# Kernel optimization log

Measured on AMD Instinct MI355X. Metric: run time of the kernel, lower is better.

The kernel has to match this reference:

```python
import jax, jax.numpy as jnp
import numpy as np

N = 100000      # nodes
E = 600000      # edges
IN = 128        # in_dim
HID = 32        # hidden_dim per head (layer 1)
HEADS = 4       # num_heads (layer 1)
NEG_SLOPE = 0.2 # PyG GATConv default negative_slope


def setup_inputs() -> dict:
    key = jax.random.key(0)
    ks = jax.random.split(key, 10)
    x = jax.random.normal(ks[0], (N, IN), dtype=jnp.float32)
    edge_index = jax.random.randint(ks[1], (2, E), 0, N, dtype=jnp.int64)
    # layer 1 params: W1 [IN, HEADS*HID], attention vectors [HEADS, HID], bias [HEADS*HID]
    W1 = jax.random.normal(ks[2], (IN, HEADS * HID), dtype=jnp.float32) / np.float32(np.sqrt(IN))
    att_src1 = jax.random.normal(ks[3], (HEADS, HID), dtype=jnp.float32) * 0.1
    att_dst1 = jax.random.normal(ks[4], (HEADS, HID), dtype=jnp.float32) * 0.1
    b1 = jnp.zeros((HEADS * HID,), dtype=jnp.float32)
    # layer 2 params: heads=1, out channels=1, concat=False
    W2 = jax.random.normal(ks[5], (HEADS * HID, 1), dtype=jnp.float32) / np.float32(np.sqrt(HEADS * HID))
    att_src2 = jax.random.normal(ks[6], (1, 1), dtype=jnp.float32) * 0.1
    att_dst2 = jax.random.normal(ks[7], (1, 1), dtype=jnp.float32) * 0.1
    b2 = jnp.zeros((1,), dtype=jnp.float32)
    return {"x": x, "edge_index": edge_index, "W1": W1, "att_src1": att_src1,
            "att_dst1": att_dst1, "b1": b1, "W2": W2, "att_src2": att_src2,
            "att_dst2": att_dst2, "b2": b2}


def gat_layer(x, src, dst, W, a_src, a_dst, b, heads, ch, concat):
    """PyG GATConv (eval mode): edge score + segment softmax + scatter aggregate."""
    n = x.shape[0]
    h = (x @ W).reshape(n, heads, ch)                    # [N,H,C]
    e_src = jnp.einsum('nhc,hc->nh', h, a_src)           # alpha_src per node
    e_dst = jnp.einsum('nhc,hc->nh', h, a_dst)           # alpha_dst per node
    e = jax.nn.leaky_relu(e_src[src] + e_dst[dst], NEG_SLOPE)  # [E,H]
    m = jax.ops.segment_max(e, dst, num_segments=n)      # stable softmax per dst
    p = jnp.exp(e - m[dst])
    denom = jax.ops.segment_sum(p, dst, num_segments=n)
    alpha = p / (denom[dst] + 1e-16)                     # [E,H]
    out = jax.ops.segment_sum(alpha[:, :, None] * h[src], dst, num_segments=n)  # [N,H,C]
    out = out.reshape(n, heads * ch) if concat else out.mean(axis=1)
    return out + b


def reference(x, edge_index, W1, att_src1, att_dst1, b1, W2, att_src2, att_dst2, b2):
    n = x.shape[0]
    loops = jnp.arange(n, dtype=edge_index.dtype)        # PyG add_self_loops=True
    src = jnp.concatenate([edge_index[0], loops])
    dst = jnp.concatenate([edge_index[1], loops])
    h1 = gat_layer(x, src, dst, W1, att_src1, att_dst1, b1, HEADS, HID, True)   # [N, HEADS*HID]
    out = gat_layer(h1, src, dst, W2, att_src2, att_dst2, b2, 1, 1, False)      # [N, 1]
    return out
```

## Files before the change

### kernel.cpp

```cpp
#include <hip/hip_runtime.h>
#include <hip/hip_fp16.h>
#include <math.h>

#define N_NODES 100000
#define E_EDGES 600000
#define IN_DIM  128
#define HID     32
#define HEADS   4
#define NEG     0.2f
#define CAP     32

typedef __attribute__((ext_vector_type(8))) _Float16 f16x8;
typedef __attribute__((ext_vector_type(4))) float f32x4;

__device__ __forceinline__ float lrelu(float v) { return v > 0.f ? v : NEG * v; }

#define SWZ(r, byteoff) ((byteoff) ^ (((r) & 7) << 4))


__global__ __launch_bounds__(128) void wprep_kernel(const float* __restrict__ W1,
                                                    const float* __restrict__ as1,
                                                    const float* __restrict__ ad1,
                                                    __half* __restrict__ wtx,
                                                    int* __restrict__ cnt) {
    int tid = blockIdx.x * 128 + threadIdx.x;
    for (int i = tid; i < N_NODES; i += 144 * 128) cnt[i] = 0;

    int b = blockIdx.x;
    int t = threadIdx.x;
    float v;
    if (b < 128) {
        v = W1[t * 128 + b];
    } else if (b < 136) {
        int h = b - 128;
        int hh = h & 3;
        const float* av = (h < 4) ? (as1 + hh * 32) : (ad1 + hh * 32);
        float s = 0.f;
        #pragma unroll 8
        for (int c = 0; c < 32; ++c) s += W1[t * 128 + hh * 32 + c] * av[c];
        v = s;
    } else {
        v = 0.f;
    }
    wtx[b * 128 + t] = __float2half(v);
}


__global__ __launch_bounds__(256) void gemm1_kernel(const float* __restrict__ x,
                                                    const __half* __restrict__ wtx,
                                                    __half* __restrict__ h1h,
                                                    float* __restrict__ aab) {
    __shared__ __half lx[64 * 128];
    __shared__ __half lw[144 * 128];
    int t = threadIdx.x;
    int row0 = blockIdx.x * 64;

    #pragma unroll
    for (int it = 0; it < 9; ++it) {
        int idx = t + it * 256;
        int r = idx >> 4, c = idx & 15;
        uint4 v = ((const uint4*)wtx)[idx];
        *(uint4*)((char*)lw + SWZ(r, r * 256 + c * 16)) = v;
    }
    #pragma unroll
    for (int it = 0; it < 8; ++it) {
        int idx = t + it * 256;
        int r = idx >> 5, c = idx & 31;
        int gr = row0 + r;
        float4 v = make_float4(0.f, 0.f, 0.f, 0.f);
        if (gr < N_NODES) v = ((const float4*)x)[gr * 32 + c];
        union { uint2 u; __half2 h[2]; } pk;
        pk.h[0] = __floats2half2_rn(v.x, v.y);
        pk.h[1] = __floats2half2_rn(v.z, v.w);
        *(uint2*)((char*)lx + SWZ(r, r * 256 + c * 8)) = pk.u;
    }
    __syncthreads();

    int w = t >> 6, lane = t & 63;
    int li = lane & 15, g = lane >> 4;
    int arow = w * 16 + li;

    f16x8 af[4];
    #pragma unroll
    for (int kt = 0; kt < 4; ++kt)
        af[kt] = *(const f16x8*)((const char*)lx + SWZ(arow, arow * 256 + kt * 64 + g * 16));

    f32x4 acc[9];
    #pragma unroll
    for (int ct = 0; ct < 9; ++ct) acc[ct] = (f32x4){0.f, 0.f, 0.f, 0.f};

    #pragma unroll
    for (int ct = 0; ct < 9; ++ct) {
        int n = ct * 16 + li;
        #pragma unroll
        for (int kt = 0; kt < 4; ++kt) {
            f16x8 bf = *(const f16x8*)((const char*)lw + SWZ(n, n * 256 + kt * 64 + g * 16));
            acc[ct] = __builtin_amdgcn_mfma_f32_16x16x32_f16(af[kt], bf, acc[ct], 0, 0, 0);
        }
    }

    int gr0 = row0 + w * 16 + g * 4;
    #pragma unroll
    for (int ct = 0; ct < 8; ++ct) {
        int col = ct * 16 + li;
        #pragma unroll
        for (int q = 0; q < 4; ++q) {
            int gr = gr0 + q;
            if (gr < N_NODES) h1h[gr * 128 + col] = __float2half(acc[ct][q]);
        }
    }
    if (li < 8) {
        #pragma unroll
        for (int q = 0; q < 4; ++q) {
            int gr = gr0 + q;
            if (gr < N_NODES) aab[gr * 8 + li] = acc[8][q];
        }
    }
}


__global__ __launch_bounds__(256) void scatter_kernel(const int* __restrict__ ei,
                                                      const float* __restrict__ aab,
                                                      int* __restrict__ cnt,
                                                      uint4* __restrict__ edges) {
    int e = blockIdx.x * 256 + threadIdx.x;
    if (e >= E_EDGES) return;
    int s = ei[e];
    int d = ei[E_EDGES + e];
    int slot = atomicAdd(&cnt[d], 1);
    if (slot >= CAP) return;
    float4 asv = *(const float4*)&aab[s * 8];
    float4 adv = *(const float4*)&aab[d * 8 + 4];
    float p0 = __expf(lrelu(asv.x + adv.x));
    float p1 = __expf(lrelu(asv.y + adv.y));
    float p2 = __expf(lrelu(asv.z + adv.z));
    float p3 = __expf(lrelu(asv.w + adv.w));
    union { __half2 h; unsigned u; } a, b;
    a.h = __floats2half2_rn(p0, p1);
    b.h = __floats2half2_rn(p2, p3);
    uint4 rec;
    rec.x = (unsigned)s; rec.y = a.u; rec.z = b.u; rec.w = 0;
    edges[d * CAP + slot] = rec;
}


__global__ __launch_bounds__(256) void agg1_kernel(const __half* __restrict__ h1h,
                                                   const float* __restrict__ aab,
                                                   const int* __restrict__ cnt,
                                                   const uint4* __restrict__ edges,
                                                   const float* __restrict__ b1,
                                                   const float* __restrict__ W2,
                                                   const float* __restrict__ att_src2,
                                                   const float* __restrict__ att_dst2,
                                                   float* __restrict__ h2,
                                                   float* __restrict__ a2s,
                                                   float* __restrict__ a2d) {
    int lane = threadIdx.x & 63;
    int n = blockIdx.x * 4 + (threadIdx.x >> 6);
    int g = lane >> 4;
    int c = lane & 15;
    int head = c >> 2;
    int deg = min(cnt[n], CAP);
    const uint4* eb = edges + n * CAP;

    __half2 acc01 = __half2(0.f, 0.f), acc23 = acc01, acc45 = acc01, acc67 = acc01;
    float den = 0.f;

    for (int i = 0; i < deg; i += 4) {
        int e = i + g;
        bool valid = e < deg;
        uint4 rec = eb[valid ? e : 0];
        int s = valid ? (int)rec.x : n;
        union { unsigned u; __half2 h; } py;
        py.u = (head & 2) ? rec.z : rec.y;
        __half ph = (head & 1) ? __high2half(py.h) : __low2half(py.h);
        if (!valid) ph = __half(0.f);
        __half2 pp = __half2half2(ph);
        union { uint4 u; __half2 h[4]; } hv;
        hv.u = *(const uint4*)&h1h[s * 128 + c * 8];
        acc01 = __hfma2(pp, hv.h[0], acc01);
        acc23 = __hfma2(pp, hv.h[1], acc23);
        acc45 = __hfma2(pp, hv.h[2], acc45);
        acc67 = __hfma2(pp, hv.h[3], acc67);
        den += __half2float(ph);
    }

    union { unsigned u; __half2 h; } t0, t1, t2, t3;
    #pragma unroll
    for (int m = 16; m <= 32; m <<= 1) {
        t0.u = __shfl_xor(*(unsigned*)&acc01, m, 64);
        t1.u = __shfl_xor(*(unsigned*)&acc23, m, 64);
        t2.u = __shfl_xor(*(unsigned*)&acc45, m, 64);
        t3.u = __shfl_xor(*(unsigned*)&acc67, m, 64);
        acc01 = __hadd2(acc01, t0.h);
        acc23 = __hadd2(acc23, t1.h);
        acc45 = __hadd2(acc45, t2.h);
        acc67 = __hadd2(acc67, t3.h);
        den += __shfl_xor(den, m, 64);
    }

    float s0 = __low2float(acc01), s1 = __high2float(acc01);
    float s2 = __low2float(acc23), s3 = __high2float(acc23);
    float s4 = __low2float(acc45), s5 = __high2float(acc45);
    float s6 = __low2float(acc67), s7 = __high2float(acc67);

    {
        float p = __expf(lrelu(aab[n * 8 + head] + aab[n * 8 + 4 + head]));
        union { uint4 u; __half2 h[4]; } hv;
        hv.u = *(const uint4*)&h1h[n * 128 + c * 8];
        float2 f0 = __half22float2(hv.h[0]), f1 = __half22float2(hv.h[1]);
        float2 f2 = __half22float2(hv.h[2]), f3 = __half22float2(hv.h[3]);
        s0 += p * f0.x; s1 += p * f0.y; s2 += p * f1.x; s3 += p * f1.y;
        s4 += p * f2.x; s5 += p * f2.y; s6 += p * f3.x; s7 += p * f3.y;
        den += p;
    }

    float inv = 1.f / (den + 1e-16f);
    float4 bv0 = ((const float4*)b1)[c * 2];
    float4 bv1 = ((const float4*)b1)[c * 2 + 1];
    float o0 = s0 * inv + bv0.x, o1 = s1 * inv + bv0.y;
    float o2 = s2 * inv + bv0.z, o3 = s3 * inv + bv0.w;
    float o4 = s4 * inv + bv1.x, o5 = s5 * inv + bv1.y;
    float o6 = s6 * inv + bv1.z, o7 = s7 * inv + bv1.w;

    float4 wv0 = ((const float4*)W2)[c * 2];
    float4 wv1 = ((const float4*)W2)[c * 2 + 1];
    float pp = o0 * wv0.x + o1 * wv0.y + o2 * wv0.z + o3 * wv0.w
             + o4 * wv1.x + o5 * wv1.y + o6 * wv1.z + o7 * wv1.w;
    #pragma unroll
    for (int m = 1; m <= 8; m <<= 1) pp += __shfl_xor(pp, m, 64);
    if (lane == 0) {
        h2[n] = pp;
        a2s[n] = pp * att_src2[0];
        a2d[n] = pp * att_dst2[0];
    }
}


__global__ __launch_bounds__(256) void agg2_kernel(const float* __restrict__ h2,
                                                   const float* __restrict__ a2s,
                                                   const float* __restrict__ a2d,
                                                   const int* __restrict__ cnt,
                                                   const uint4* __restrict__ edges,
                                                   const float* __restrict__ b2,
                                                   float* __restrict__ out) {
    int n = blockIdx.x * 256 + threadIdx.x;
    if (n >= N_NODES) return;
    float adn = a2d[n];
    int deg = min(cnt[n], CAP);
    const uint4* eb = edges + n * CAP;
    float num = 0.f, den = 0.f;
    for (int i = 0; i < deg; i += 4) {
        int s[4]; bool val[4]; float as_[4], hs[4];
        #pragma unroll
        for (int j = 0; j < 4; ++j) {
            val[j] = (i + j) < deg;
            s[j] = val[j] ? (int)eb[i + j].x : n;
        }
        #pragma unroll
        for (int j = 0; j < 4; ++j) as_[j] = a2s[s[j]];
        #pragma unroll
        for (int j = 0; j < 4; ++j) hs[j] = h2[s[j]];
        #pragma unroll
        for (int j = 0; j < 4; ++j) {
            float p = val[j] ? __expf(lrelu(as_[j] + adn)) : 0.f;
            num += p * hs[j];
            den += p;
        }
    }
    {
        float p = __expf(lrelu(a2s[n] + adn));
        num += p * h2[n];
        den += p;
    }
    out[n] = num / (den + 1e-16f) + b2[0];
}


extern "C" void kernel_launch(void* const* d_in, const int* in_sizes, int n_in,
                              void* d_out, int out_size, void* d_ws, size_t ws_size,
                              hipStream_t stream) {
    const float* x        = (const float*)d_in[0];
    const int*   ei       = (const int*)d_in[1];
    const float* W1       = (const float*)d_in[2];
    const float* att_src1 = (const float*)d_in[3];
    const float* att_dst1 = (const float*)d_in[4];
    const float* b1       = (const float*)d_in[5];
    const float* W2       = (const float*)d_in[6];
    const float* att_src2 = (const float*)d_in[7];
    const float* att_dst2 = (const float*)d_in[8];
    const float* b2       = (const float*)d_in[9];
    float* out = (float*)d_out;

    char* ws = (char*)d_ws;
    size_t off = 0;
    auto alloc = [&](size_t bytes) {
        char* p = ws + off;
        off = (off + bytes + 255) & ~(size_t)255;
        return p;
    };
    __half* h1h    = (__half*)alloc((size_t)N_NODES * 128 * 2);
    float*  aab    = (float*)alloc((size_t)N_NODES * 8 * 4);
    __half* wtx    = (__half*)alloc((size_t)144 * 128 * 2);
    float*  h2     = (float*)alloc((size_t)N_NODES * 4);
    float*  a2s    = (float*)alloc((size_t)N_NODES * 4);
    float*  a2d    = (float*)alloc((size_t)N_NODES * 4);
    int*    cnt    = (int*)alloc((size_t)N_NODES * 4);
    uint4*  edges  = (uint4*)alloc((size_t)N_NODES * CAP * 16);

    const int NB_NODE = (N_NODES + 255) / 256;
    const int NB_EDGE = (E_EDGES + 255) / 256;
    const int NB_WAVE = (N_NODES + 3) / 4;
    const int NB_GEMM = (N_NODES + 63) / 64;

    wprep_kernel<<<144, 128, 0, stream>>>(W1, att_src1, att_dst1, wtx, cnt);
    gemm1_kernel<<<NB_GEMM, 256, 0, stream>>>(x, wtx, h1h, aab);
    scatter_kernel<<<NB_EDGE, 256, 0, stream>>>(ei, aab, cnt, edges);
    agg1_kernel<<<NB_WAVE, 256, 0, stream>>>(h1h, aab, cnt, edges,
                                             b1, W2, att_src2, att_dst2,
                                             h2, a2s, a2d);
    agg2_kernel<<<NB_NODE, 256, 0, stream>>>(h2, a2s, a2d, cnt, edges, b2, out);
}
```

Baseline: 211.2 us.

## Assign one 16-lane group per node in agg1 instead of a full wave

The first-layer aggregation now maps 16 lanes to each destination node, so each wave handles four nodes, instead of splitting one node's edges across four 16-lane groups. Each group walks its node's edge list serially. This removes the cross-group shuffle reduction and the masking for partial edge batches, and launches a quarter as many blocks. In exchange each node's edges are processed one at a time, with less memory-level parallelism per node, and lanes in a wave diverge when neighbouring nodes have different degrees.

```diff
diff --git a/kernel.cpp b/kernel.cpp
--- a/kernel.cpp
+++ b/kernel.cpp
@@ -155,26 +155,22 @@
                                                    float* __restrict__ h2,
                                                    float* __restrict__ a2s,
                                                    float* __restrict__ a2d) {
-    int lane = threadIdx.x & 63;
-    int n = blockIdx.x * 4 + (threadIdx.x >> 6);
-    int g = lane >> 4;
-    int c = lane & 15;
+    int tid = threadIdx.x;
+    int c = tid & 15;
+    int n = blockIdx.x * 16 + (tid >> 4);
     int head = c >> 2;
     int deg = min(cnt[n], CAP);
-    const uint4* eb = edges + n * CAP;
+    const uint4* eb = edges + (size_t)n * CAP;
 
     __half2 acc01 = __half2(0.f, 0.f), acc23 = acc01, acc45 = acc01, acc67 = acc01;
     float den = 0.f;
 
-    for (int i = 0; i < deg; i += 4) {
-        int e = i + g;
-        bool valid = e < deg;
-        uint4 rec = eb[valid ? e : 0];
-        int s = valid ? (int)rec.x : n;
+    for (int e = 0; e < deg; ++e) {
+        uint4 rec = eb[e];
+        int s = (int)rec.x;
         union { unsigned u; __half2 h; } py;
         py.u = (head & 2) ? rec.z : rec.y;
         __half ph = (head & 1) ? __high2half(py.h) : __low2half(py.h);
-        if (!valid) ph = __half(0.f);
         __half2 pp = __half2half2(ph);
         union { uint4 u; __half2 h[4]; } hv;
         hv.u = *(const uint4*)&h1h[s * 128 + c * 8];
@@ -183,20 +179,6 @@
         acc45 = __hfma2(pp, hv.h[2], acc45);
         acc67 = __hfma2(pp, hv.h[3], acc67);
         den += __half2float(ph);
-    }
-
-    union { unsigned u; __half2 h; } t0, t1, t2, t3;
-    #pragma unroll
-    for (int m = 16; m <= 32; m <<= 1) {
-        t0.u = __shfl_xor(*(unsigned*)&acc01, m, 64);
-        t1.u = __shfl_xor(*(unsigned*)&acc23, m, 64);
-        t2.u = __shfl_xor(*(unsigned*)&acc45, m, 64);
-        t3.u = __shfl_xor(*(unsigned*)&acc67, m, 64);
-        acc01 = __hadd2(acc01, t0.h);
-        acc23 = __hadd2(acc23, t1.h);
-        acc45 = __hadd2(acc45, t2.h);
-        acc67 = __hadd2(acc67, t3.h);
-        den += __shfl_xor(den, m, 64);
     }
 
     float s0 = __low2float(acc01), s1 = __high2float(acc01);
@@ -229,7 +211,7 @@
              + o4 * wv1.x + o5 * wv1.y + o6 * wv1.z + o7 * wv1.w;
     #pragma unroll
     for (int m = 1; m <= 8; m <<= 1) pp += __shfl_xor(pp, m, 64);
-    if (lane == 0) {
+    if (c == 0) {
         h2[n] = pp;
         a2s[n] = pp * att_src2[0];
         a2d[n] = pp * att_dst2[0];
@@ -248,7 +230,7 @@
     if (n >= N_NODES) return;
     float adn = a2d[n];
     int deg = min(cnt[n], CAP);
-    const uint4* eb = edges + n * CAP;
+    const uint4* eb = edges + (size_t)n * CAP;
     float num = 0.f, den = 0.f;
     for (int i = 0; i < deg; i += 4) {
         int s[4]; bool val[4]; float as_[4], hs[4];
@@ -310,13 +292,13 @@
 
     const int NB_NODE = (N_NODES + 255) / 256;
     const int NB_EDGE = (E_EDGES + 255) / 256;
-    const int NB_WAVE = (N_NODES + 3) / 4;
+    const int NB_AGG1 = N_NODES / 16;
     const int NB_GEMM = (N_NODES + 63) / 64;
 
     wprep_kernel<<<144, 128, 0, stream>>>(W1, att_src1, att_dst1, wtx, cnt);
     gemm1_kernel<<<NB_GEMM, 256, 0, stream>>>(x, wtx, h1h, aab);
     scatter_kernel<<<NB_EDGE, 256, 0, stream>>>(ei, aab, cnt, edges);
-    agg1_kernel<<<NB_WAVE, 256, 0, stream>>>(h1h, aab, cnt, edges,
+    agg1_kernel<<<NB_AGG1, 256, 0, stream>>>(h1h, aab, cnt, edges,
                                              b1, W2, att_src2, att_dst2,
                                              h2, a2s, a2d);
     agg2_kernel<<<NB_NODE, 256, 0, stream>>>(h2, a2s, a2d, cnt, edges, b2, out);
```

Result: faster. 202.1 us (-4.3%).
